# Performance work log

Measured on AMD Instinct MI355X. Metric: run time of the kernel, lower is better.

## Reference

```python
import jax, jax.numpy as jnp
import numpy as np

D_MODEL = 1024
NUM_HEADS = 16
D_K = D_MODEL // NUM_HEADS


def setup_inputs() -> dict:
    key = jax.random.key(0)
    ks = jax.random.split(key, 9)
    B, S = 2, 2048
    s = 1.0 / np.sqrt(D_MODEL)
    return {
        "x": jax.random.normal(ks[0], (B, S, D_MODEL), dtype=jnp.float32),
        "Wq": jax.random.normal(ks[1], (D_MODEL, D_MODEL), dtype=jnp.float32) * s,
        "bq": jnp.zeros((D_MODEL,), dtype=jnp.float32),
        "Wk": jax.random.normal(ks[2], (D_MODEL, D_MODEL), dtype=jnp.float32) * s,
        "bk": jnp.zeros((D_MODEL,), dtype=jnp.float32),
        "Wv": jax.random.normal(ks[3], (D_MODEL, D_MODEL), dtype=jnp.float32) * s,
        "bv": jnp.zeros((D_MODEL,), dtype=jnp.float32),
        "Wo": jax.random.normal(ks[4], (D_MODEL, D_MODEL), dtype=jnp.float32) * s,
        "bo": jnp.zeros((D_MODEL,), dtype=jnp.float32),
    }


def reference(x, Wq, bq, Wk, bk, Wv, bv, Wo, bo):
    B, S, _ = x.shape
    # project and split heads: [B, H, S, d_k]
    def proj(W, b):
        return (x @ W + b).reshape(B, S, NUM_HEADS, D_K).transpose(0, 2, 1, 3)
    Q, K, V = proj(Wq, bq), proj(Wk, bk), proj(Wv, bv)
    scores = jnp.einsum("bhqd,bhkd->bhqk", Q, K) / jnp.sqrt(jnp.float32(D_K))
    causal = jnp.tril(jnp.ones((S, S), dtype=bool))
    scores = jnp.where(causal[None, None], scores, jnp.float32(-1e9))
    attn = jax.nn.softmax(scores, axis=-1)  # dropout=0 (eval)
    out = jnp.einsum("bhqk,bhkd->bhqd", attn, V)
    out = out.transpose(0, 2, 1, 3).reshape(B, S, D_MODEL)
    return out @ Wo + bo
```

## Files before the change

### kernel.cpp

```cpp
#include <hip/hip_runtime.h>

#define SEQ    2048
#define NH     16
#define DMODEL 1024

typedef __attribute__((ext_vector_type(4)))  float f32x4;
typedef __attribute__((ext_vector_type(8)))  short s16x8;
typedef __attribute__((ext_vector_type(4)))  short s16x4;
typedef __attribute__((ext_vector_type(2)))  unsigned u32x2;

__device__ __forceinline__ float bf2f(unsigned short u){
  union { unsigned int i; float f; } v; v.i = ((unsigned int)u) << 16; return v.f;
}
__device__ __forceinline__ unsigned short f2bf(float f){
  union { float f; unsigned int i; } v; v.f = f;
  unsigned int r = v.i + 0x7fffu + ((v.i >> 16) & 1u);
  return (unsigned short)(r >> 16);
}
__device__ __forceinline__ unsigned short f2bf_hu(float f){
  union { float f; unsigned int i; } v; v.f = f;
  return (unsigned short)((v.i + 0x8000u) >> 16);
}
__device__ __forceinline__ float fast_exp2(float x){
  return __builtin_amdgcn_exp2f(x);
}
__device__ __forceinline__ void gld_lds16(const void* g, void* l){
  __builtin_amdgcn_global_load_lds((const __attribute__((address_space(1))) void*)g,
                                   (__attribute__((address_space(3))) void*)l,
                                   16, 0, 0);
}

__global__ __launch_bounds__(256) void k_cast_x(const float* __restrict__ x,
                                                unsigned short* __restrict__ hi){
  int i = blockIdx.x * 256 + threadIdx.x;
  f32x4 v = ((const f32x4*)x)[i];
  s16x4 h;
  #pragma unroll
  for (int j = 0; j < 4; ++j) h[j] = (short)f2bf(v[j]);
  ((s16x4*)hi)[i] = h;
}

__global__ __launch_bounds__(256) void k_t_w(const float* __restrict__ W0,
                                             const float* __restrict__ W1,
                                             const float* __restrict__ W2,
                                             const float* __restrict__ W3,
                                             unsigned short* __restrict__ Wt){
  __shared__ float t[64][65];
  const float* Ws[4] = {W0, W1, W2, W3};
  const float* W = Ws[blockIdx.z];
  const int n0 = blockIdx.x * 64, k0 = blockIdx.y * 64;
  const int tid = threadIdx.x;
  #pragma unroll
  for (int i = 0; i < 16; ++i){
    int e = i * 256 + tid;
    int r = e >> 6, c = e & 63;
    t[r][c] = W[(size_t)(k0 + r) * 1024 + n0 + c];
  }
  __syncthreads();
  size_t base = ((size_t)blockIdx.z << 20);
  #pragma unroll
  for (int i = 0; i < 16; ++i){
    int e = i * 256 + tid;
    int nn = e >> 6, kk = e & 63;
    Wt[base + (size_t)(n0 + nn) * 1024 + k0 + kk] = f2bf(t[kk][nn]);
  }
}

__global__ __launch_bounds__(512, 2)
void gemm_qkv8(const unsigned short* __restrict__ A,
               const unsigned short* __restrict__ B,
               const float* __restrict__ bq, const float* __restrict__ bk,
               const float* __restrict__ bv,
               unsigned short* __restrict__ Qb, unsigned short* __restrict__ Kb,
               unsigned short* __restrict__ Vt)
{
  __shared__ __align__(16) unsigned short lA[2][256 * 64];
  __shared__ __align__(16) unsigned short lB[2][192 * 64];
  const int tid = threadIdx.x;
  const int lane = tid & 63, w = tid >> 6;
  const int wm = w >> 2, wn = w & 3;
  const int lr = lane & 15, lq = lane >> 4;
  const int m0 = blockIdx.y * 256, n0 = blockIdx.x * 192;

  size_t asrc[4]; unsigned adst[4];
  #pragma unroll
  for (int p = 0; p < 4; ++p){
    int c = p * 512 + tid;
    int row = c >> 3, lc = (c & 7) ^ (row & 7);
    asrc[p] = (size_t)(m0 + row) * 1024 + lc * 8;
    adst[p] = c * 8;
  }
  size_t bsrc[3]; unsigned bdst[3];
  #pragma unroll
  for (int p = 0; p < 3; ++p){
    int c = p * 512 + tid;
    int row = c >> 3, lc = (c & 7) ^ (row & 7);
    bsrc[p] = (size_t)(n0 + row) * 1024 + lc * 8;
    bdst[p] = c * 8;
  }
  auto stage = [&](int buf, int k0){
    #pragma unroll
    for (int p = 0; p < 4; ++p) gld_lds16(A + asrc[p] + k0, &lA[buf][adst[p]]);
    #pragma unroll
    for (int p = 0; p < 3; ++p) gld_lds16(B + bsrc[p] + k0, &lB[buf][bdst[p]]);
  };

  const int csw0 = ((0 + lq) ^ (lr & 7)) << 4;
  const int csw1 = ((4 + lq) ^ (lr & 7)) << 4;

  f32x4 acc[8][3];
  #pragma unroll
  for (int i = 0; i < 8; ++i)
    #pragma unroll
    for (int j = 0; j < 3; ++j) acc[i][j] = (f32x4)0.0f;

  stage(0, 0);
  stage(1, 64);
  asm volatile("s_waitcnt vmcnt(7)" ::: "memory");
  __builtin_amdgcn_sched_barrier(0);
  __builtin_amdgcn_s_barrier();
  __builtin_amdgcn_sched_barrier(0);

  for (int t = 0; t < 16; ++t){
    const int p = t & 1;
    s16x8 fa[8][2], fb[3][2];
    {
      const char* baseA = (const char*)&lA[p][0];
      const char* baseB = (const char*)&lB[p][0];
      #pragma unroll
      for (int mf = 0; mf < 8; ++mf){
        const char* pr = baseA + (wm * 128 + mf * 16 + lr) * 128;
        fa[mf][0] = *(const s16x8*)(pr + csw0);
        fa[mf][1] = *(const s16x8*)(pr + csw1);
      }
      #pragma unroll
      for (int nf = 0; nf < 3; ++nf){
        const char* pr = baseB + (wn * 48 + nf * 16 + lr) * 128;
        fb[nf][0] = *(const s16x8*)(pr + csw0);
        fb[nf][1] = *(const s16x8*)(pr + csw1);
      }
    }
    asm volatile("s_waitcnt lgkmcnt(0)" ::: "memory");
    __builtin_amdgcn_sched_barrier(0);
    __builtin_amdgcn_s_barrier();
    __builtin_amdgcn_sched_barrier(0);
    if (t + 2 < 16) stage(p, (t + 2) * 64);
    #pragma unroll
    for (int kk = 0; kk < 2; ++kk)
      #pragma unroll
      for (int mf = 0; mf < 8; ++mf)
        #pragma unroll
        for (int nf = 0; nf < 3; ++nf)
          acc[mf][nf] = __builtin_amdgcn_mfma_f32_16x16x32_bf16(fa[mf][kk], fb[nf][kk], acc[mf][nf], 0, 0, 0);
    __builtin_amdgcn_sched_barrier(0);
    if (t < 14) asm volatile("s_waitcnt vmcnt(7)" ::: "memory");
    else        asm volatile("s_waitcnt vmcnt(0)" ::: "memory");
    __builtin_amdgcn_sched_barrier(0);
    __builtin_amdgcn_s_barrier();
    __builtin_amdgcn_sched_barrier(0);
  }

  const int mb = m0 + wm * 128, nb = n0 + wn * 48;
  #pragma unroll
  for (int mf = 0; mf < 8; ++mf){
    int row = mb + mf * 16 + lq * 4;
    #pragma unroll
    for (int nf = 0; nf < 3; ++nf){
      int col = nb + nf * 16 + lr;
      int mat = col >> 10, cm = col & 1023;
      float bs = ((mat == 0) ? bq : (mat == 1) ? bk : bv)[cm];
      if (mat < 2){
        unsigned short* QK = mat ? Kb : Qb;
        #pragma unroll
        for (int r = 0; r < 4; ++r)
          QK[(size_t)(row + r) * 1024 + cm] = f2bf(acc[mf][nf][r] + bs);
      } else {
        int bb = row >> 11, s = row & 2047;
        int h = cm >> 6, d = cm & 63;
        s16x4 pk;
        #pragma unroll
        for (int r = 0; r < 4; ++r) pk[r] = (short)f2bf(acc[mf][nf][r] + bs);
        *(s16x4*)&Vt[(((size_t)(bb * NH + h) * 64 + d) << 11) + s] = pk;
      }
    }
  }
}

__global__ __launch_bounds__(256, 2)
void gemm_o(const unsigned short* __restrict__ A,
            const unsigned short* __restrict__ B,
            const float* __restrict__ bias,
            float* __restrict__ C)
{
  __shared__ __align__(16) unsigned short lA[2][64 * 32];
  __shared__ __align__(16) unsigned short lB[2][128 * 32];
  const int tid = threadIdx.x;
  const int lane = tid & 63, w = tid >> 6;
  const int wm = w >> 1, wn = w & 1;
  const int lr = lane & 15, lq = lane >> 4;
  const int m0 = blockIdx.y * 64, n0 = blockIdx.x * 128;

  auto stage = [&](int buf, int k0){
    {
      int c = tid;
      int row = c >> 2, cc = c & 3;
      gld_lds16(A + (size_t)(m0 + row) * 1024 + k0 + cc * 8, &lA[buf][c * 8]);
    }
    #pragma unroll
    for (int it = 0; it < 2; ++it){
      int c = it * 256 + tid;
      int row = c >> 2, cc = c & 3;
      gld_lds16(B + (size_t)(n0 + row) * 1024 + k0 + cc * 8, &lB[buf][c * 8]);
    }
  };

  f32x4 acc[2][4];
  #pragma unroll
  for (int i = 0; i < 2; ++i)
    #pragma unroll
    for (int j = 0; j < 4; ++j) acc[i][j] = (f32x4)0.0f;

  stage(0, 0);
  __syncthreads();
  for (int k0 = 0; k0 < 1024; k0 += 32){
    const int cur = (k0 >> 5) & 1;
    if (k0 + 32 < 1024) stage(cur ^ 1, k0 + 32);
    s16x8 fa[2], fb[4];
    #pragma unroll
    for (int f = 0; f < 2; ++f)
      fa[f] = *(const s16x8*)&lA[cur][(wm * 32 + f * 16 + lr) * 32 + lq * 8];
    #pragma unroll
    for (int f = 0; f < 4; ++f)
      fb[f] = *(const s16x8*)&lB[cur][(wn * 64 + f * 16 + lr) * 32 + lq * 8];
    #pragma unroll
    for (int i = 0; i < 2; ++i)
      #pragma unroll
      for (int j = 0; j < 4; ++j)
        acc[i][j] = __builtin_amdgcn_mfma_f32_16x16x32_bf16(fa[i], fb[j], acc[i][j], 0, 0, 0);
    __syncthreads();
  }

  const int mb = m0 + wm * 32, nb = n0 + wn * 64;
  #pragma unroll
  for (int i = 0; i < 2; ++i){
    int row = mb + i * 16 + lq * 4;
    #pragma unroll
    for (int j = 0; j < 4; ++j){
      int col = nb + j * 16 + lr;
      float bs = bias[col];
      #pragma unroll
      for (int r = 0; r < 4; ++r)
        C[(size_t)(row + r) * 1024 + col] = acc[i][j][r] + bs;
    }
  }
}

__global__ __launch_bounds__(256, 4)
void attn_fwd(const unsigned short* __restrict__ Qg,
              const unsigned short* __restrict__ Kg,
              const unsigned short* __restrict__ Vtg,
              unsigned short* __restrict__ Oh)
{
  __shared__ __align__(16) unsigned short lK[2][64 * 64];
  __shared__ __align__(16) unsigned short lV[2][64 * 64];
  __shared__ __align__(16) unsigned short lP[4][16 * 64];
  const int tid = threadIdx.x;
  const int lane = tid & 63, w = tid >> 6;
  const int lr = lane & 15, lq = lane >> 4;
  const int bh = blockIdx.x;
  const int b = bh >> 4, h = bh & 15;
  const int qt = 31 - blockIdx.y;
  const int qrow = qt * 64 + w * 16;

  const float qscale = 0.125f * 1.44269504088896f;
  const float FIXMAX = 11.0f;

  const unsigned short* qp = Qg + (size_t)(b * SEQ + qrow + lr) * 1024 + h * 64 + lq * 8;
  s16x8 q0 = *(const s16x8*)qp;
  s16x8 q1 = *(const s16x8*)(qp + 32);
  #pragma unroll
  for (int j = 0; j < 8; ++j){
    q0[j] = (short)f2bf(bf2f((unsigned short)q0[j]) * qscale);
    q1[j] = (short)f2bf(bf2f((unsigned short)q1[j]) * qscale);
  }

  float ls = 0.f;
  f32x4 accO[4];
  #pragma unroll
  for (int dt = 0; dt < 4; ++dt) accO[dt] = (f32x4)0.0f;

  auto stage = [&](int buf, int kt){
    const int kc0 = kt * 64;
    #pragma unroll
    for (int it = 0; it < 2; ++it){
      int c = it * 256 + tid;
      int row = c >> 3, sc = c & 7;
      int lc = sc ^ (row & 7);
      gld_lds16(Kg + (size_t)(b * SEQ + kc0 + row) * 1024 + h * 64 + lc * 8, &lK[buf][c * 8]);
      gld_lds16(Vtg + ((size_t)(bh * 64 + row) << 11) + kc0 + lc * 8, &lV[buf][c * 8]);
    }
  };

  stage(0, 0);
  if (qt > 0){
    stage(1, 1);
    asm volatile("s_waitcnt vmcnt(4)" ::: "memory");
  } else {
    asm volatile("s_waitcnt vmcnt(0)" ::: "memory");
  }
  __builtin_amdgcn_sched_barrier(0);
  __builtin_amdgcn_s_barrier();
  __builtin_amdgcn_sched_barrier(0);

  for (int kt = 0; kt <= qt; ++kt){
    const int cur = kt & 1;
    const bool diag = (kt == qt);

    s16x8 kf[4][2], vf[4][2];
    #pragma unroll
    for (int st = 0; st < 4; ++st){
      int tok = st * 16 + lr;
      const char* kb = (const char*)&lK[cur][0] + tok * 128;
      kf[st][0] = *(const s16x8*)(kb + (((0 + lq) ^ (tok & 7)) << 4));
      kf[st][1] = *(const s16x8*)(kb + (((4 + lq) ^ (tok & 7)) << 4));
      const char* vb = (const char*)&lV[cur][0] + tok * 128;
      vf[st][0] = *(const s16x8*)(vb + (((0 + lq) ^ (tok & 7)) << 4));
      vf[st][1] = *(const s16x8*)(vb + (((4 + lq) ^ (tok & 7)) << 4));
    }
    asm volatile("s_waitcnt lgkmcnt(0)" ::: "memory");
    __builtin_amdgcn_sched_barrier(0);
    __builtin_amdgcn_s_barrier();
    __builtin_amdgcn_sched_barrier(0);
    if (kt + 2 <= qt) stage(cur, kt + 2);

    f32x4 s4[4];
    #pragma unroll
    for (int st = 0; st < 4; ++st){
      if (diag && st > w){ s4[st] = (f32x4)(-1e30f); continue; }
      f32x4 z = (f32x4)0.0f;
      z = __builtin_amdgcn_mfma_f32_16x16x32_bf16(kf[st][0], q0, z, 0, 0, 0);
      z = __builtin_amdgcn_mfma_f32_16x16x32_bf16(kf[st][1], q1, z, 0, 0, 0);
      if (diag && st == w){
        #pragma unroll
        for (int r = 0; r < 4; ++r)
          if (lq * 4 + r > lr) z[r] = -1e30f;
      }
      s4[st] = z;
    }

    char* pb = (char*)&lP[w][0];
    #pragma unroll
    for (int st = 0; st < 4; ++st){
      float p0 = fast_exp2(s4[st][0] - FIXMAX);
      float p1 = fast_exp2(s4[st][1] - FIXMAX);
      float p2 = fast_exp2(s4[st][2] - FIXMAX);
      float p3 = fast_exp2(s4[st][3] - FIXMAX);
      ls += (p0 + p1) + (p2 + p3);
      u32x2 d;
      d[0] = ((unsigned)f2bf_hu(p1) << 16) | f2bf_hu(p0);
      d[1] = ((unsigned)f2bf_hu(p3) << 16) | f2bf_hu(p2);
      int base = lr * 128 + ((st * 32 + lq * 8) ^ ((lr & 7) << 4));
      *(u32x2*)(pb + base) = d;
    }
    asm volatile("s_waitcnt lgkmcnt(0)" ::: "memory");
    __builtin_amdgcn_sched_barrier(0);
    s16x8 pf0 = *(const s16x8*)(pb + lr * 128 + (((0 + lq) << 4) ^ ((lr & 7) << 4)));
    s16x8 pf1 = *(const s16x8*)(pb + lr * 128 + (((4 + lq) << 4) ^ ((lr & 7) << 4)));

    #pragma unroll
    for (int dt = 0; dt < 4; ++dt){
      accO[dt] = __builtin_amdgcn_mfma_f32_16x16x32_bf16(pf0, vf[dt][0], accO[dt], 0, 0, 0);
      accO[dt] = __builtin_amdgcn_mfma_f32_16x16x32_bf16(pf1, vf[dt][1], accO[dt], 0, 0, 0);
    }
    __builtin_amdgcn_sched_barrier(0);
    if (kt + 2 <= qt)      asm volatile("s_waitcnt vmcnt(4)" ::: "memory");
    else if (kt + 1 <= qt) asm volatile("s_waitcnt vmcnt(0)" ::: "memory");
    __builtin_amdgcn_sched_barrier(0);
    __builtin_amdgcn_s_barrier();
    __builtin_amdgcn_sched_barrier(0);
  }

  float t = ls;
  t += __shfl_xor(t, 16);
  t += __shfl_xor(t, 32);
  #pragma unroll
  for (int r = 0; r < 4; ++r){
    float rn = 1.0f / __shfl(t, lq * 4 + r);
    #pragma unroll
    for (int dt = 0; dt < 4; ++dt){
      size_t off = (size_t)(b * SEQ + qrow + lq * 4 + r) * 1024 + h * 64 + dt * 16 + lr;
      Oh[off] = f2bf(accO[dt][r] * rn);
    }
  }
}

extern "C" void kernel_launch(void* const* d_in, const int* in_sizes, int n_in,
                              void* d_out, int out_size, void* d_ws, size_t ws_size,
                              hipStream_t stream){
  (void)in_sizes; (void)n_in; (void)out_size; (void)ws_size;
  const float* x  = (const float*)d_in[0];
  const float* Wq = (const float*)d_in[1];
  const float* bq = (const float*)d_in[2];
  const float* Wk = (const float*)d_in[3];
  const float* bk = (const float*)d_in[4];
  const float* Wv = (const float*)d_in[5];
  const float* bv = (const float*)d_in[6];
  const float* Wo = (const float*)d_in[7];
  const float* bo = (const float*)d_in[8];

  const size_t NT = 4096;
  unsigned short* xh  = (unsigned short*)d_ws;
  unsigned short* wt  = xh + NT * 1024;
  unsigned short* Qb  = wt + 4u * 1024 * 1024;
  unsigned short* Kb  = Qb + NT * 1024;
  unsigned short* Vt  = Kb + NT * 1024;
  unsigned short* Ohb = Vt + NT * 1024;

  k_cast_x<<<4096, 256, 0, stream>>>(x, xh);
  k_t_w<<<dim3(16, 16, 4), 256, 0, stream>>>(Wq, Wk, Wv, Wo, wt);

  gemm_qkv8<<<dim3(16, 16), 512, 0, stream>>>(xh, wt, bq, bk, bv, Qb, Kb, Vt);

  attn_fwd<<<dim3(32, 32), 256, 0, stream>>>(Qb, Kb, Vt, Ohb);

  const size_t WM = (size_t)1024 * 1024;
  gemm_o<<<dim3(8, 64), 256, 0, stream>>>(Ohb, wt + 3 * WM, bo, (float*)d_out);
}
```

Baseline: 105.7 us.

## Restructure output GEMM with K=64 tiles, XOR-swizzled LDS, and 2-deep prefetch

The output projection GEMM now stages 64-wide K tiles instead of 32, with an XOR swizzle on LDS column chunks to avoid bank conflicts. Two stages are kept in flight through explicit vmcnt waits and raw barriers, replacing the per-iteration __syncthreads. This aims to cut barrier count and LDS conflicts and to hide global-load latency, at the cost of doubled LDS use (48KB) and fragile hand-written waitcnt scheduling.

```diff
diff --git a/kernel.cpp b/kernel.cpp
--- a/kernel.cpp
+++ b/kernel.cpp
@@ -187,57 +187,95 @@
 }
 
 __global__ __launch_bounds__(256, 2)
-void gemm_o(const unsigned short* __restrict__ A,
-            const unsigned short* __restrict__ B,
-            const float* __restrict__ bias,
-            float* __restrict__ C)
+void gemm_o8(const unsigned short* __restrict__ A,
+             const unsigned short* __restrict__ B,
+             const float* __restrict__ bias,
+             float* __restrict__ C)
 {
-  __shared__ __align__(16) unsigned short lA[2][64 * 32];
-  __shared__ __align__(16) unsigned short lB[2][128 * 32];
+  __shared__ __align__(16) unsigned short lA[2][64 * 64];
+  __shared__ __align__(16) unsigned short lB[2][128 * 64];
   const int tid = threadIdx.x;
   const int lane = tid & 63, w = tid >> 6;
   const int wm = w >> 1, wn = w & 1;
   const int lr = lane & 15, lq = lane >> 4;
   const int m0 = blockIdx.y * 64, n0 = blockIdx.x * 128;
 
+  size_t asrc[2]; unsigned adst[2];
+  #pragma unroll
+  for (int p = 0; p < 2; ++p){
+    int c = p * 256 + tid;
+    int row = c >> 3, lc = (c & 7) ^ (row & 7);
+    asrc[p] = (size_t)(m0 + row) * 1024 + lc * 8;
+    adst[p] = c * 8;
+  }
+  size_t bsrc[4]; unsigned bdst[4];
+  #pragma unroll
+  for (int p = 0; p < 4; ++p){
+    int c = p * 256 + tid;
+    int row = c >> 3, lc = (c & 7) ^ (row & 7);
+    bsrc[p] = (size_t)(n0 + row) * 1024 + lc * 8;
+    bdst[p] = c * 8;
+  }
   auto stage = [&](int buf, int k0){
+    #pragma unroll
+    for (int p = 0; p < 2; ++p) gld_lds16(A + asrc[p] + k0, &lA[buf][adst[p]]);
+    #pragma unroll
+    for (int p = 0; p < 4; ++p) gld_lds16(B + bsrc[p] + k0, &lB[buf][bdst[p]]);
+  };
+
+  const int csw0 = ((0 + lq) ^ (lr & 7)) << 4;
+  const int csw1 = ((4 + lq) ^ (lr & 7)) << 4;
+
+  f32x4 acc[2][4];
+  #pragma unroll
+  for (int i = 0; i < 2; ++i)
+    #pragma unroll
+    for (int j = 0; j < 4; ++j) acc[i][j] = (f32x4)0.0f;
+
+  stage(0, 0);
+  stage(1, 64);
+  asm volatile("s_waitcnt vmcnt(6)" ::: "memory");
+  __builtin_amdgcn_sched_barrier(0);
+  __builtin_amdgcn_s_barrier();
+  __builtin_amdgcn_sched_barrier(0);
+
+  for (int t = 0; t < 16; ++t){
+    const int p = t & 1;
+    s16x8 fa[2][2], fb[4][2];
     {
-      int c = tid;
-      int row = c >> 2, cc = c & 3;
-      gld_lds16(A + (size_t)(m0 + row) * 1024 + k0 + cc * 8, &lA[buf][c * 8]);
-    }
-    #pragma unroll
-    for (int it = 0; it < 2; ++it){
-      int c = it * 256 + tid;
-      int row = c >> 2, cc = c & 3;
-      gld_lds16(B + (size_t)(n0 + row) * 1024 + k0 + cc * 8, &lB[buf][c * 8]);
-    }
-  };
-
-  f32x4 acc[2][4];
-  #pragma unroll
-  for (int i = 0; i < 2; ++i)
-    #pragma unroll
-    for (int j = 0; j < 4; ++j) acc[i][j] = (f32x4)0.0f;
-
-  stage(0, 0);
-  __syncthreads();
-  for (int k0 = 0; k0 < 1024; k0 += 32){
-    const int cur = (k0 >> 5) & 1;
-    if (k0 + 32 < 1024) stage(cur ^ 1, k0 + 32);
-    s16x8 fa[2], fb[4];
-    #pragma unroll
-    for (int f = 0; f < 2; ++f)
-      fa[f] = *(const s16x8*)&lA[cur][(wm * 32 + f * 16 + lr) * 32 + lq * 8];
-    #pragma unroll
-    for (int f = 0; f < 4; ++f)
-      fb[f] = *(const s16x8*)&lB[cur][(wn * 64 + f * 16 + lr) * 32 + lq * 8];
-    #pragma unroll
-    for (int i = 0; i < 2; ++i)
-      #pragma unroll
-      for (int j = 0; j < 4; ++j)
-        acc[i][j] = __builtin_amdgcn_mfma_f32_16x16x32_bf16(fa[i], fb[j], acc[i][j], 0, 0, 0);
-    __syncthreads();
+      const char* baseA = (const char*)&lA[p][0];
+      const char* baseB = (const char*)&lB[p][0];
+      #pragma unroll
+      for (int mf = 0; mf < 2; ++mf){
+        const char* pr = baseA + (wm * 32 + mf * 16 + lr) * 128;
+        fa[mf][0] = *(const s16x8*)(pr + csw0);
+        fa[mf][1] = *(const s16x8*)(pr + csw1);
+      }
+      #pragma unroll
+      for (int nf = 0; nf < 4; ++nf){
+        const char* pr = baseB + (wn * 64 + nf * 16 + lr) * 128;
+        fb[nf][0] = *(const s16x8*)(pr + csw0);
+        fb[nf][1] = *(const s16x8*)(pr + csw1);
+      }
+    }
+    asm volatile("s_waitcnt lgkmcnt(0)" ::: "memory");
+    __builtin_amdgcn_sched_barrier(0);
+    __builtin_amdgcn_s_barrier();
+    __builtin_amdgcn_sched_barrier(0);
+    if (t + 2 < 16) stage(p, (t + 2) * 64);
+    #pragma unroll
+    for (int kk = 0; kk < 2; ++kk)
+      #pragma unroll
+      for (int i = 0; i < 2; ++i)
+        #pragma unroll
+        for (int j = 0; j < 4; ++j)
+          acc[i][j] = __builtin_amdgcn_mfma_f32_16x16x32_bf16(fa[i][kk], fb[j][kk], acc[i][j], 0, 0, 0);
+    __builtin_amdgcn_sched_barrier(0);
+    if (t < 14) asm volatile("s_waitcnt vmcnt(6)" ::: "memory");
+    else        asm volatile("s_waitcnt vmcnt(0)" ::: "memory");
+    __builtin_amdgcn_sched_barrier(0);
+    __builtin_amdgcn_s_barrier();
+    __builtin_amdgcn_sched_barrier(0);
   }
 
   const int mb = m0 + wm * 32, nb = n0 + wn * 64;
@@ -424,5 +462,5 @@
   attn_fwd<<<dim3(32, 32), 256, 0, stream>>>(Qb, Kb, Vt, Ohb);
 
   const size_t WM = (size_t)1024 * 1024;
-  gemm_o<<<dim3(8, 64), 256, 0, stream>>>(Ohb, wt + 3 * WM, bo, (float*)d_out);
-}
+  gemm_o8<<<dim3(8, 64), 256, 0, stream>>>(Ohb, wt + 3 * WM, bo, (float*)d_out);
+}
```

Result: faster. 99.47 us (-5.9%).
